# Performance work log

Hardware: AMD Instinct MI355X
Metric: run time of the kernel (lower is better)

## Reference

```python
import jax, jax.numpy as jnp
import numpy as np

D_MODEL = 1024
M = 64            # oscillators; state dim N = 2*M
N = 2 * M
N_H = 2           # Householder reflections per step
DT = 0.1
OMEGA_MAX = 100.0
BATCH, SEQ = 8, 2048


def setup_inputs() -> dict:
    key = jax.random.key(0)
    ks = jax.random.split(key, 8)
    u = jax.random.normal(ks[0], (BATCH, SEQ, D_MODEL), jnp.float32)
    # learned parameters (scaled like the module's small-gain init)
    W_A = jax.random.normal(ks[1], (M, D_MODEL), jnp.float32) * 0.01
    b_A = jnp.zeros((M,), jnp.float32)
    W_k = jax.random.normal(ks[2], (N_H, N, D_MODEL), jnp.float32) * 0.02
    b_k = jnp.zeros((N_H, N), jnp.float32)
    W_beta = jax.random.normal(ks[3], (N_H, D_MODEL), jnp.float32) * 0.02
    b_beta = jnp.zeros((N_H,), jnp.float32)
    B_w = jax.random.normal(ks[4], (N, D_MODEL), jnp.float32) * 0.02
    B_b = jnp.zeros((N,), jnp.float32)
    C = jax.random.normal(ks[5], (D_MODEL, N), jnp.float32) * 0.01
    D = jax.random.normal(ks[6], (D_MODEL,), jnp.float32) * 0.01
    return dict(u=u, W_A=W_A, b_A=b_A, W_k=W_k, b_k=b_k,
                W_beta=W_beta, b_beta=b_beta, B_w=B_w, B_b=B_b, C=C, D=D)


def reference(u, W_A, b_A, W_k, b_k, W_beta, b_beta, B_w, B_b, C, D):
    batch = u.shape[0]
    # --- precompute all input-dependent per-step quantities as big GEMMs ---
    A = jax.nn.relu(jnp.einsum('btd,md->btm', u, W_A) + b_A)
    A = jnp.minimum(A, OMEGA_MAX)                       # clamp(max=omega_max)
    S = 1.0 / (1.0 + (DT * DT) * A)                     # (B,T,M)
    K = jnp.einsum('btd,jnd->btjn', u, W_k) + b_k       # (B,T,n_h,N)
    K = K / jnp.maximum(jnp.linalg.norm(K, axis=-1, keepdims=True), 1e-12)
    beta = 2.0 * jax.nn.sigmoid(jnp.einsum('btd,jd->btj', u, W_beta) + b_beta)
    Bt = jnp.einsum('btd,nd->btn', u, B_w) + B_b        # (B,T,N)

    # time-major for scan
    xs = (jnp.moveaxis(A, 1, 0), jnp.moveaxis(S, 1, 0), jnp.moveaxis(K, 1, 0),
          jnp.moveaxis(beta, 1, 0), jnp.moveaxis(Bt, 1, 0))
    h0 = jnp.zeros((batch, N), u.dtype)

    def step(h, x):
        A_t, S_t, K_t, beta_t, B_t = x
        # oscillatory rotation-contraction R_t @ h (m 2x2 blocks)
        z, y = h[:, :M], h[:, M:]
        z_new = S_t * z - DT * A_t * S_t * y
        y_new = DT * S_t * z + S_t * y
        h = jnp.concatenate([z_new, y_new], axis=-1)
        # sequential Householder product H_t @ h (fixed small n_h loop)
        for j in range(N_H):
            k = K_t[:, j]                                # (B,N), unit norm
            dot = jnp.sum(k * h, axis=-1, keepdims=True)
            h = h - beta_t[:, j:j + 1] * k * dot
        h = h + B_t
        return h, h

    _, hs = jax.lax.scan(step, h0, xs)                  # (T,B,N)
    hs = jnp.moveaxis(hs, 0, 1)                         # (B,T,N)
    return jnp.einsum('btn,dn->btd', hs, C) + u * D
```

## Files before the change

### kernel.cpp

```cpp
#include <hip/hip_runtime.h>
#include <cmath>


#define NTOK 16384
#define TT 2048
#define BB 8
#define DM 1024
#define FS 520
#define CH 64
#define LCH 32
#define NCH 512
#define NW 448
#define NWP 512

typedef short bf16x8 __attribute__((ext_vector_type(8)));
typedef float f32x4 __attribute__((ext_vector_type(4)));

#define GLOAD_LDS16(g, l)                                          \
  __builtin_amdgcn_global_load_lds(                                \
      (const __attribute__((address_space(1))) void*)(g),          \
      (__attribute__((address_space(3))) void*)(l), 16, 0, 0)

#define RAW_BAR() do {                                             \
    asm volatile("s_waitcnt lgkmcnt(0)" ::: "memory");             \
    __builtin_amdgcn_sched_barrier(0);                             \
    __builtin_amdgcn_s_barrier();                                  \
    __builtin_amdgcn_sched_barrier(0);                             \
  } while (0)

#define WAIT_VM(N) do {                                            \
    __builtin_amdgcn_sched_barrier(0);                             \
    asm volatile("s_waitcnt vmcnt(" #N ")" ::: "memory");          \
    __builtin_amdgcn_sched_barrier(0);                             \
  } while (0)

__global__ __launch_bounds__(256) void packW(
    const float* __restrict__ W_A, const float* __restrict__ b_A,
    const float* __restrict__ W_k, const float* __restrict__ b_k,
    const float* __restrict__ b_beta,
    const float* __restrict__ B_w, const float* __restrict__ B_b,
    float* __restrict__ Wp, float* __restrict__ bias) {
  int r = blockIdx.x;
  int tid = threadIdx.x;
  const float* src;
  float bv;
  if (r < 64)       { src = W_A + (size_t)r * DM;         bv = b_A[r]; }
  else if (r < 320) { src = W_k + (size_t)(r - 64) * DM;  bv = b_k[r - 64]; }
  else              { src = B_w + (size_t)(r - 320) * DM; bv = B_b[r - 320]; }
  ((float4*)(Wp + (size_t)r * DM))[tid] = ((const float4*)src)[tid];
  if (tid == 0) bias[r] = bv;
  if (r == 0 && tid < 2) bias[448 + tid] = b_beta[tid];
}

__device__ inline unsigned short bf16_rne(float x) {
  unsigned b = __float_as_uint(x);
  b += 0x7FFFu + ((b >> 16) & 1u);
  return (unsigned short)(b >> 16);
}

__device__ inline void split_bf16(float x, unsigned short& h, unsigned short& l) {
  unsigned b = __float_as_uint(x);
  h = (unsigned short)(b >> 16);
  float rem = x - __uint_as_float(b & 0xFFFF0000u);
  l = bf16_rne(rem);
}

__global__ __launch_bounds__(256) void convertU(
    const float* __restrict__ u, unsigned short* __restrict__ uh,
    unsigned short* __restrict__ ul) {
  int gid = blockIdx.x * 256 + threadIdx.x;
  int m = gid >> 8;
  int g = gid & 255;
  float4 v = *(const float4*)(u + (size_t)m * DM + g * 4);
  int kt = g >> 3, gg = g & 7;
  int p = gg & 3, h = gg >> 2;
  int mr = m & 127, mb = m >> 7;
  int pp = p ^ ((mr >> 2) & 3);
  size_t dst = ((size_t)(mb * 32 + kt)) * 4096 + mr * 32 + ((pp << 1) | h) * 4;
  ushort4 hi, lo;
  split_bf16(v.x, hi.x, lo.x);
  split_bf16(v.y, hi.y, lo.y);
  split_bf16(v.z, hi.z, lo.z);
  split_bf16(v.w, hi.w, lo.w);
  *(ushort4*)(uh + dst) = hi;
  *(ushort4*)(ul + dst) = lo;
}

__global__ __launch_bounds__(256) void convertW(
    const float* __restrict__ Wp, unsigned short* __restrict__ Wb) {
  int gid = blockIdx.x * 256 + threadIdx.x;
  int n = gid >> 8, g = gid & 255;
  int kt = g >> 3, gg = g & 7;
  int p = gg & 3, h = gg >> 2;
  int nr = n & 127, nb = n >> 7;
  int pp = p ^ ((nr >> 2) & 3);
  size_t dst = ((size_t)(nb * 32 + kt)) * 4096 + nr * 32 + ((pp << 1) | h) * 4;
  ushort4 hv = make_ushort4(0, 0, 0, 0);
  if (n < NW) {
    float4 v = *(const float4*)(Wp + (size_t)n * DM + g * 4);
    hv.x = bf16_rne(v.x); hv.y = bf16_rne(v.y);
    hv.z = bf16_rne(v.z); hv.w = bf16_rne(v.w);
  }
  *(ushort4*)(Wb + dst) = hv;
}

__global__ __launch_bounds__(256) void convertC(
    const float* __restrict__ Cm, unsigned short* __restrict__ Chp,
    unsigned short* __restrict__ Clp) {
  int gid = blockIdx.x * 256 + threadIdx.x;
  int d = gid >> 5;
  int g = gid & 31;
  float4 v = *(const float4*)(Cm + (size_t)d * 128 + g * 4);
  int kt = g >> 3, gg = g & 7;
  int p = gg & 3, h = gg >> 2;
  int nr = d & 127, nb = d >> 7;
  int pp = p ^ ((nr >> 2) & 3);
  size_t dst = ((size_t)(nb * 4 + kt)) * 4096 + nr * 32 + ((pp << 1) | h) * 4;
  ushort4 hi, lo;
  split_bf16(v.x, hi.x, lo.x);
  split_bf16(v.y, hi.y, lo.y);
  split_bf16(v.z, hi.z, lo.z);
  split_bf16(v.w, hi.w, lo.w);
  *(ushort4*)(Chp + dst) = hi;
  *(ushort4*)(Clp + dst) = lo;
}

__global__ __launch_bounds__(256) void gemmA_mfma(
    const unsigned short* __restrict__ uh, const unsigned short* __restrict__ ul,
    const unsigned short* __restrict__ Wb, float* __restrict__ Feat) {
  __shared__ __align__(16) unsigned short As[8192];
  __shared__ __align__(16) unsigned short Bs[8192];
  const int tid = threadIdx.x;
  const int wv = tid >> 6, ln = tid & 63;
  const int lr = ln & 15, G = ln >> 4;
  const int wm = wv >> 1, wn = wv & 1;
  const int x = G ^ (lr >> 2);
  f32x4 acc[4][4];
#pragma unroll
  for (int i = 0; i < 4; ++i)
#pragma unroll
    for (int j = 0; j < 4; ++j) acc[i][j] = (f32x4){0.f, 0.f, 0.f, 0.f};

  const size_t aBase = (size_t)blockIdx.x * 32 * 4096;
  const size_t bBase = (size_t)blockIdx.y * 32 * 4096;
  const int so = wv * 512 + ln * 8;
  const int ld = wv * 512;

  auto stage = [&](int step, int buf) {
    const unsigned short* pa = (step < 32) ? uh : ul;
    const int kt = step & 31;
    const unsigned short* ga = pa + aBase + (size_t)kt * 4096;
    const unsigned short* gb = Wb + bBase + (size_t)kt * 4096;
    unsigned short* A = As + buf * 4096;
    unsigned short* B = Bs + buf * 4096;
    GLOAD_LDS16(ga + so,        A + ld);
    GLOAD_LDS16(ga + 2048 + so, A + 2048 + ld);
    GLOAD_LDS16(gb + so,        B + ld);
    GLOAD_LDS16(gb + 2048 + so, B + 2048 + ld);
  };

  stage(0, 0);
  __syncthreads();
  for (int s = 0; s < 64; ++s) {
    const int cur = s & 1;
    if (s + 1 < 64) stage(s + 1, cur ^ 1);
    bf16x8 af[4], bfr[4];
    const char* Ab = (const char*)(As + cur * 4096) + ((wm * 64 + lr) << 6) + (x << 4);
    const char* Bb = (const char*)(Bs + cur * 4096) + ((wn * 64 + lr) << 6) + (x << 4);
#pragma unroll
    for (int i = 0; i < 4; ++i) {
      af[i]  = *(const bf16x8*)(Ab + i * 1024);
      bfr[i] = *(const bf16x8*)(Bb + i * 1024);
    }
#pragma unroll
    for (int i = 0; i < 4; ++i)
#pragma unroll
      for (int j = 0; j < 4; ++j)
        acc[i][j] = __builtin_amdgcn_mfma_f32_16x16x32_bf16(
            af[i], bfr[j], acc[i][j], 0, 0, 0);
    __syncthreads();
  }
  const int row0 = (blockIdx.x << 7) + wm * 64 + (G << 2);
  const int col0 = (blockIdx.y << 7) + wn * 64 + lr;
  float* fb = Feat + (size_t)row0 * FS + col0;
#pragma unroll
  for (int i = 0; i < 4; ++i)
#pragma unroll
    for (int j = 0; j < 4; ++j) {
      float* d = fb + (size_t)(i * 16) * FS + j * 16;
#pragma unroll
      for (int r = 0; r < 4; ++r) d[(size_t)r * FS] = acc[i][j][r];
    }
}

__global__ __launch_bounds__(256) void gemmC_mfma(
    const unsigned short* __restrict__ hsh, const unsigned short* __restrict__ hsl,
    const unsigned short* __restrict__ Chp, const unsigned short* __restrict__ Clp,
    const float* __restrict__ u, const float* __restrict__ Dv,
    float* __restrict__ out) {
  __shared__ __align__(16) unsigned short As[8192];
  __shared__ __align__(16) unsigned short Bs[8192];
  const int tid = threadIdx.x;
  const int wv = tid >> 6, ln = tid & 63;
  const int lr = ln & 15, G = ln >> 4;
  const int wm = wv >> 1, wn = wv & 1;
  const int x = G ^ (lr >> 2);
  f32x4 acc[4][4];
#pragma unroll
  for (int i = 0; i < 4; ++i)
#pragma unroll
    for (int j = 0; j < 4; ++j) acc[i][j] = (f32x4){0.f, 0.f, 0.f, 0.f};

  const size_t aBase = (size_t)blockIdx.x * 4 * 4096;
  const size_t bBase = (size_t)blockIdx.y * 4 * 4096;
  const int so = wv * 512 + ln * 8;
  const int ld = wv * 512;

  auto stage = [&](int step, int buf) {
    const int pass = step >> 2, kt = step & 3;
    const unsigned short* pa = (pass == 1) ? hsl : hsh;
    const unsigned short* pb = (pass == 2) ? Clp : Chp;
    const unsigned short* ga = pa + aBase + (size_t)kt * 4096;
    const unsigned short* gb = pb + bBase + (size_t)kt * 4096;
    unsigned short* A = As + buf * 4096;
    unsigned short* B = Bs + buf * 4096;
    GLOAD_LDS16(ga + so,        A + ld);
    GLOAD_LDS16(ga + 2048 + so, A + 2048 + ld);
    GLOAD_LDS16(gb + so,        B + ld);
    GLOAD_LDS16(gb + 2048 + so, B + 2048 + ld);
  };

  stage(0, 0);
  __syncthreads();
  for (int s = 0; s < 12; ++s) {
    const int cur = s & 1;
    if (s + 1 < 12) stage(s + 1, cur ^ 1);
    bf16x8 af[4], bfr[4];
    const char* Ab = (const char*)(As + cur * 4096) + ((wm * 64 + lr) << 6) + (x << 4);
    const char* Bb = (const char*)(Bs + cur * 4096) + ((wn * 64 + lr) << 6) + (x << 4);
#pragma unroll
    for (int i = 0; i < 4; ++i) {
      af[i]  = *(const bf16x8*)(Ab + i * 1024);
      bfr[i] = *(const bf16x8*)(Bb + i * 1024);
    }
#pragma unroll
    for (int i = 0; i < 4; ++i)
#pragma unroll
      for (int j = 0; j < 4; ++j)
        acc[i][j] = __builtin_amdgcn_mfma_f32_16x16x32_bf16(
            af[i], bfr[j], acc[i][j], 0, 0, 0);
    __syncthreads();
  }
  const int row0 = (blockIdx.x << 7) + wm * 64 + (G << 2);
  const int col0 = (blockIdx.y << 7) + wn * 64 + lr;
#pragma unroll
  for (int j = 0; j < 4; ++j) {
    float dv = Dv[col0 + j * 16];
#pragma unroll
    for (int i = 0; i < 4; ++i) {
#pragma unroll
      for (int r = 0; r < 4; ++r) {
        size_t off = (size_t)(row0 + i * 16 + r) * DM + col0 + j * 16;
        out[off] = fmaf(u[off], dv, acc[i][j][r]);
      }
    }
  }
}

__device__ inline float wave_sum(float v) {
#pragma unroll
  for (int off = 32; off > 0; off >>= 1) v += __shfl_xor(v, off, 64);
  return v;
}

__global__ __launch_bounds__(64) void postA(float* __restrict__ Feat,
                                            const float* __restrict__ bias,
                                            const float* __restrict__ u,
                                            const float* __restrict__ Wb) {
  const int t = blockIdx.x, lane = threadIdx.x;
  float* f = Feat + (size_t)t * FS;
  float s0 = 0.f, s1 = 0.f;
#pragma unroll
  for (int j = 0; j < 4; ++j) {
    float4 uv = *(const float4*)(u + (size_t)t * DM + j * 256 + lane * 4);
    float4 w0 = *(const float4*)(Wb + j * 256 + lane * 4);
    float4 w1 = *(const float4*)(Wb + DM + j * 256 + lane * 4);
    s0 = fmaf(uv.x, w0.x, s0); s0 = fmaf(uv.y, w0.y, s0);
    s0 = fmaf(uv.z, w0.z, s0); s0 = fmaf(uv.w, w0.w, s0);
    s1 = fmaf(uv.x, w1.x, s1); s1 = fmaf(uv.y, w1.y, s1);
    s1 = fmaf(uv.z, w1.z, s1); s1 = fmaf(uv.w, w1.w, s1);
  }
  s0 = wave_sum(s0); s1 = wave_sum(s1);
  float a = f[lane] + bias[lane];
  a = fminf(fmaxf(a, 0.f), 100.f);
  float S = 1.f / (1.f + 0.01f * a);
  f[lane] = S;
  f[448 + lane] = 0.1f * a * S;
  float k10 = f[64 + lane] + bias[64 + lane];
  float k11 = f[128 + lane] + bias[128 + lane];
  float n1 = wave_sum(k10 * k10 + k11 * k11);
  float inv1 = 1.f / fmaxf(sqrtf(n1), 1e-12f);
  k10 *= inv1; k11 *= inv1;
  f[64 + lane] = k10; f[128 + lane] = k11;
  float k20 = f[192 + lane] + bias[192 + lane];
  float k21 = f[256 + lane] + bias[256 + lane];
  float n2 = wave_sum(k20 * k20 + k21 * k21);
  float inv2 = 1.f / fmaxf(sqrtf(n2), 1e-12f);
  k20 *= inv2; k21 *= inv2;
  f[192 + lane] = k20; f[256 + lane] = k21;
  float c12 = wave_sum(k10 * k20 + k11 * k21);
  if (lane == 0) {
    f[512] = 2.f / (1.f + expf(-(s0 + bias[448])));
    f[513] = 2.f / (1.f + expf(-(s1 + bias[449])));
    f[514] = c12;
  }
  f[320 + lane] += bias[320 + lane];
  f[384 + lane] += bias[384 + lane];
}

__global__ __launch_bounds__(1024, 8) void scanB01(
    const float* __restrict__ Feat, float* __restrict__ Mc,
    float* __restrict__ dc) {
  const int bid = blockIdx.x;
  const int tid = threadIdx.x;
  __shared__ float fb[2][4 * FS];

  if (bid < NCH / 16) {
    const int cid = bid * 16 + (tid >> 6);
    const int lane = tid & 63;
    float z = 0.f, y = 0.f;
    const int t0 = (cid >> 6) * TT + (cid & 63) * LCH;
    for (int t = t0; t < t0 + LCH; ++t) {
      const float* __restrict__ f = Feat + (size_t)t * FS;
      float s = f[lane], c1 = f[448 + lane];
      float k1z = f[64 + lane], k1y = f[128 + lane];
      float k2z = f[192 + lane], k2y = f[256 + lane];
      float bz = f[320 + lane], by = f[384 + lane];
      float b1 = f[512], b2 = f[513], c12 = f[514];
      float sz = s * z;
      float zn = fmaf(-c1, y, sz);
      float yn = fmaf(s, y, 0.1f * sz);
      float p = fmaf(k1y, yn, k1z * zn);
      float qq = fmaf(k2y, yn, k2z * zn);
#pragma unroll
      for (int off = 32; off > 0; off >>= 1) {
        p += __shfl_xor(p, off, 64);
        qq += __shfl_xor(qq, off, 64);
      }
      float e1 = b1 * p;
      float d2 = fmaf(-c12, e1, qq);
      float e2 = b2 * d2;
      z = fmaf(-e1, k1z, zn); z = fmaf(-e2, k2z, z); z += bz;
      y = fmaf(-e1, k1y, yn); y = fmaf(-e2, k2y, y); y += by;
    }
    dc[(size_t)cid * 128 + lane] = z;
    dc[(size_t)cid * 128 + 64 + lane] = y;
    return;
  }

  const int cid = bid - NCH / 16;
  const int t0 = (cid >> 6) * TT + (cid & 63) * LCH;
  const int col = tid >> 3, q = tid & 7;
  const int i0 = q * 8;
  float mz[8], my[8];
#pragma unroll
  for (int j = 0; j < 8; ++j) {
    mz[j] = (i0 + j == col) ? 1.f : 0.f;
    my[j] = (64 + i0 + j == col) ? 1.f : 0.f;
  }
  {
    const float4* src = (const float4*)(Feat + (size_t)t0 * FS);
    if (tid < FS) ((float4*)fb[0])[tid] = src[tid];
  }
  __syncthreads();
  for (int g = 0; g < LCH / 4; ++g) {
    const int cur = g & 1;
    float4 pf0;
    const bool pre = (g < LCH / 4 - 1) && (tid < FS);
    if (pre) {
      const float4* src = (const float4*)(Feat + (size_t)(t0 + (g + 1) * 4) * FS);
      pf0 = src[tid];
    }
#pragma unroll
    for (int s = 0; s < 4; ++s) {
      const float* f = fb[cur] + s * FS;
      float sj[8], cj[8], k1z[8], k1y[8], k2z[8], k2y[8];
#pragma unroll
      for (int v = 0; v < 2; ++v) {
        *(float4*)&sj[4 * v]  = *(const float4*)(f + i0 + 4 * v);
        *(float4*)&cj[4 * v]  = *(const float4*)(f + 448 + i0 + 4 * v);
        *(float4*)&k1z[4 * v] = *(const float4*)(f + 64 + i0 + 4 * v);
        *(float4*)&k1y[4 * v] = *(const float4*)(f + 128 + i0 + 4 * v);
        *(float4*)&k2z[4 * v] = *(const float4*)(f + 192 + i0 + 4 * v);
        *(float4*)&k2y[4 * v] = *(const float4*)(f + 256 + i0 + 4 * v);
      }
      float4 sc = *(const float4*)(f + 512);
      float p0 = 0.f, p1 = 0.f, r0 = 0.f, r1 = 0.f;
#pragma unroll
      for (int j = 0; j < 8; ++j) {
        float s0 = sj[j], c1 = cj[j];
        float z = mz[j], y = my[j];
        float sz = s0 * z;
        z = fmaf(-c1, y, sz);
        y = fmaf(s0, y, 0.1f * sz);
        mz[j] = z; my[j] = y;
        if (j & 1) {
          p1 = fmaf(k1z[j], z, p1); p1 = fmaf(k1y[j], y, p1);
          r1 = fmaf(k2z[j], z, r1); r1 = fmaf(k2y[j], y, r1);
        } else {
          p0 = fmaf(k1z[j], z, p0); p0 = fmaf(k1y[j], y, p0);
          r0 = fmaf(k2z[j], z, r0); r0 = fmaf(k2y[j], y, r0);
        }
      }
      float p = p0 + p1, r2 = r0 + r1;
      p  += __shfl_xor(p, 1, 64);  p  += __shfl_xor(p, 2, 64);
      p  += __shfl_xor(p, 4, 64);
      r2 += __shfl_xor(r2, 1, 64); r2 += __shfl_xor(r2, 2, 64);
      r2 += __shfl_xor(r2, 4, 64);
      float e1 = sc.x * p;
      float e2 = sc.y * fmaf(-sc.z, e1, r2);
#pragma unroll
      for (int j = 0; j < 8; ++j) {
        float z = fmaf(-e1, k1z[j], mz[j]);
        mz[j] = fmaf(-e2, k2z[j], z);
        float y = fmaf(-e1, k1y[j], my[j]);
        my[j] = fmaf(-e2, k2y[j], y);
      }
    }
    if (pre) ((float4*)fb[1 - cur])[tid] = pf0;
    __syncthreads();
  }
  float* dst = Mc + ((size_t)cid * 128 + col) * 128;
  *(float4*)(dst + i0)          = *(float4*)&mz[0];
  *(float4*)(dst + i0 + 4)      = *(float4*)&mz[4];
  *(float4*)(dst + 64 + i0)     = *(float4*)&my[0];
  *(float4*)(dst + 64 + i0 + 4) = *(float4*)&my[4];
}

__global__ __launch_bounds__(1024, 1) void scanB2(
    const float* __restrict__ Mc, const float* __restrict__ dc,
    float* __restrict__ hstart) {
  const int b = blockIdx.x;
  const int tid = threadIdx.x;
  const int i = tid & 127, jh = tid >> 7;
  const int wv = tid >> 6;
  __shared__ __align__(16) float Ms[2][16384];
  __shared__ float h[128];
  __shared__ float red[8][128];
  if (tid < 128) h[tid] = 0.f;

  auto stage = [&](int cn, int buf) {
    const float* g = Mc + (size_t)(b * CH + cn) * 16384;
#pragma unroll
    for (int q = 0; q < 4; ++q) {
      const float* gp = g + q * 4096 + wv * 256 + (tid & 63) * 4;
      float* lp = Ms[buf] + q * 4096 + wv * 256;
      GLOAD_LDS16(gp, lp);
    }
  };

  stage(0, 0);
  float d0 = dc[(size_t)(b * CH) * 128 + i];
  __syncthreads();

  int cur = 0;
  for (int c = 0; c < CH; ++c) {
    const int cn = (c + 1) & (CH - 1);
    stage(cn, cur ^ 1);
    float d1 = dc[(size_t)(b * CH + cn) * 128 + i];
    WAIT_VM(5);
    RAW_BAR();
    if (tid < 128) hstart[(size_t)(b * CH + c) * 128 + tid] = h[tid];
    float acc = 0.f;
#pragma unroll
    for (int j = 0; j < 16; ++j)
      acc = fmaf(Ms[cur][(jh * 16 + j) * 128 + i], h[jh * 16 + j], acc);
    red[jh][i] = acc;
    RAW_BAR();
    if (tid < 128) {
      float sum = d0;
#pragma unroll
      for (int k = 0; k < 8; ++k) sum += red[k][tid];
      h[tid] = sum;
    }
    d0 = d1;
    cur ^= 1;
  }
}

__global__ __launch_bounds__(64) void scanB3(
    const float* __restrict__ Feat, const float* __restrict__ hstart,
    unsigned short* __restrict__ hsh, unsigned short* __restrict__ hsl) {
  const int cid = blockIdx.x;
  const int lane = threadIdx.x;
  float z = hstart[(size_t)cid * 128 + lane];
  float y = hstart[(size_t)cid * 128 + 64 + lane];
  const int t0 = (cid >> 6) * TT + (cid & 63) * LCH;
  const int ktz = lane >> 5, kkz = lane & 31;
  const int kty = (64 + lane) >> 5;
  const int pz = (kkz >> 2) & 3, hz = kkz >> 4;
  const int lowz = kkz & 3;
  for (int t = t0; t < t0 + LCH; ++t) {
    const float* __restrict__ f = Feat + (size_t)t * FS;
    float s = f[lane], c1 = f[448 + lane];
    float k1z = f[64 + lane], k1y = f[128 + lane];
    float k2z = f[192 + lane], k2y = f[256 + lane];
    float bz = f[320 + lane], by = f[384 + lane];
    float b1 = f[512], b2 = f[513], c12 = f[514];
    float sz = s * z;
    float zn = fmaf(-c1, y, sz);
    float yn = fmaf(s, y, 0.1f * sz);
    float p = fmaf(k1y, yn, k1z * zn);
    float qq = fmaf(k2y, yn, k2z * zn);
#pragma unroll
    for (int off = 32; off > 0; off >>= 1) {
      p += __shfl_xor(p, off, 64);
      qq += __shfl_xor(qq, off, 64);
    }
    float e1 = b1 * p;
    float d2 = fmaf(-c12, e1, qq);
    float e2 = b2 * d2;
    zn = fmaf(-e1, k1z, zn); zn = fmaf(-e2, k2z, zn); zn += bz;
    yn = fmaf(-e1, k1y, yn); yn = fmaf(-e2, k2y, yn); yn += by;
    {
      const int mb = t >> 7, mr = t & 127;
      const int xr = (mr >> 2) & 3;
      size_t idxz = ((size_t)(mb * 4 + ktz)) * 4096 + mr * 32 +
                    ((((pz ^ xr) << 1) | hz)) * 4 + lowz;
      size_t idxy = ((size_t)(mb * 4 + kty)) * 4096 + mr * 32 +
                    ((((pz ^ xr) << 1) | hz)) * 4 + lowz;
      unsigned short hi, lo;
      split_bf16(zn, hi, lo);
      hsh[idxz] = hi; hsl[idxz] = lo;
      split_bf16(yn, hi, lo);
      hsh[idxy] = hi; hsl[idxy] = lo;
    }
    z = zn; y = yn;
  }
}

extern "C" void kernel_launch(void* const* d_in, const int* in_sizes, int n_in,
                              void* d_out, int out_size, void* d_ws, size_t ws_size,
                              hipStream_t stream) {
  const float* u      = (const float*)d_in[0];
  const float* W_A    = (const float*)d_in[1];
  const float* b_A    = (const float*)d_in[2];
  const float* W_k    = (const float*)d_in[3];
  const float* b_k    = (const float*)d_in[4];
  const float* W_beta = (const float*)d_in[5];
  const float* b_beta = (const float*)d_in[6];
  const float* B_w    = (const float*)d_in[7];
  const float* B_b    = (const float*)d_in[8];
  const float* Cm     = (const float*)d_in[9];
  const float* Dv     = (const float*)d_in[10];
  float* out = (float*)d_out;
  char* ws = (char*)d_ws;
  float* Wp     = (float*)(ws);
  unsigned short* Wb = (unsigned short*)(ws + 1835008);
  float* bias   = (float*)(ws + 4194304);
  float* Feat   = (float*)(ws + 4198400);
  unsigned short* uh = (unsigned short*)(ws + 38277120);
  float* Mc     = (float*)(ws + 38277120);
  unsigned short* ul = (unsigned short*)(ws + 71831552);
  unsigned short* hsh = (unsigned short*)(ws + 71831552);
  unsigned short* hsl = (unsigned short*)(ws + 76025856);
  unsigned short* Chp = (unsigned short*)(ws + 80220160);
  unsigned short* Clp = (unsigned short*)(ws + 80482304);
  float* dcv    = (float*)(ws + 80744448);
  float* hstart = (float*)(ws + 81006592);

  packW<<<dim3(448), dim3(256), 0, stream>>>(W_A, b_A, W_k, b_k, b_beta,
                                             B_w, B_b, Wp, bias);
  convertW<<<dim3(512), dim3(256), 0, stream>>>(Wp, Wb);
  convertU<<<dim3(16384), dim3(256), 0, stream>>>(u, uh, ul);
  gemmA_mfma<<<dim3(128, 4), dim3(256), 0, stream>>>(uh, ul, Wb, Feat);
  convertC<<<dim3(128), dim3(256), 0, stream>>>(Cm, Chp, Clp);
  postA<<<dim3(16384), dim3(64), 0, stream>>>(Feat, bias, u, W_beta);
  scanB01<<<dim3(NCH / 16 + NCH), dim3(1024), 0, stream>>>(Feat, Mc, dcv);
  scanB2<<<dim3(8), dim3(1024), 0, stream>>>(Mc, dcv, hstart);
  scanB3<<<dim3(NCH), dim3(64), 0, stream>>>(Feat, hstart, hsh, hsl);
  gemmC_mfma<<<dim3(128, 8), dim3(256), 0, stream>>>(hsh, hsl, Chp, Clp,
                                                     u, Dv, out);
}
```

Measured before the change: 434.9 us.

## Split chunk-scan into separate matrix and offset kernels with 16 rows per thread

Splits the fused scanB01 kernel into scanB1, which builds the per-chunk transition matrices, and scanB0, which computes the per-chunk offsets, each launched separately. scanB1 now uses 512-thread blocks where each thread owns 16 rows instead of 8. This halves the shuffle reduction depth and the thread count per chunk, at the cost of more registers per thread and a serial accumulation chain. The extra launch for scanB0 serializes work that previously shared one grid, and the higher register pressure may lower occupancy.

```diff
diff --git a/kernel.cpp b/kernel.cpp
--- a/kernel.cpp
+++ b/kernel.cpp
@@ -318,75 +318,40 @@
   f[384 + lane] += bias[384 + lane];
 }
 
-__global__ __launch_bounds__(1024, 8) void scanB01(
-    const float* __restrict__ Feat, float* __restrict__ Mc,
-    float* __restrict__ dc) {
-  const int bid = blockIdx.x;
+__global__ __launch_bounds__(512, 2) void scanB1(
+    const float* __restrict__ Feat, float* __restrict__ Mc) {
+  const int cid = blockIdx.x;
+  const int t0 = (cid >> 6) * TT + (cid & 63) * LCH;
   const int tid = threadIdx.x;
+  const int col = tid >> 2, q = tid & 3;
+  const int i0 = q * 16;
   __shared__ float fb[2][4 * FS];
-
-  if (bid < NCH / 16) {
-    const int cid = bid * 16 + (tid >> 6);
-    const int lane = tid & 63;
-    float z = 0.f, y = 0.f;
-    const int t0 = (cid >> 6) * TT + (cid & 63) * LCH;
-    for (int t = t0; t < t0 + LCH; ++t) {
-      const float* __restrict__ f = Feat + (size_t)t * FS;
-      float s = f[lane], c1 = f[448 + lane];
-      float k1z = f[64 + lane], k1y = f[128 + lane];
-      float k2z = f[192 + lane], k2y = f[256 + lane];
-      float bz = f[320 + lane], by = f[384 + lane];
-      float b1 = f[512], b2 = f[513], c12 = f[514];
-      float sz = s * z;
-      float zn = fmaf(-c1, y, sz);
-      float yn = fmaf(s, y, 0.1f * sz);
-      float p = fmaf(k1y, yn, k1z * zn);
-      float qq = fmaf(k2y, yn, k2z * zn);
-#pragma unroll
-      for (int off = 32; off > 0; off >>= 1) {
-        p += __shfl_xor(p, off, 64);
-        qq += __shfl_xor(qq, off, 64);
-      }
-      float e1 = b1 * p;
-      float d2 = fmaf(-c12, e1, qq);
-      float e2 = b2 * d2;
-      z = fmaf(-e1, k1z, zn); z = fmaf(-e2, k2z, z); z += bz;
-      y = fmaf(-e1, k1y, yn); y = fmaf(-e2, k2y, y); y += by;
-    }
-    dc[(size_t)cid * 128 + lane] = z;
-    dc[(size_t)cid * 128 + 64 + lane] = y;
-    return;
-  }
-
-  const int cid = bid - NCH / 16;
-  const int t0 = (cid >> 6) * TT + (cid & 63) * LCH;
-  const int col = tid >> 3, q = tid & 7;
-  const int i0 = q * 8;
-  float mz[8], my[8];
-#pragma unroll
-  for (int j = 0; j < 8; ++j) {
+  float mz[16], my[16];
+#pragma unroll
+  for (int j = 0; j < 16; ++j) {
     mz[j] = (i0 + j == col) ? 1.f : 0.f;
     my[j] = (64 + i0 + j == col) ? 1.f : 0.f;
   }
   {
     const float4* src = (const float4*)(Feat + (size_t)t0 * FS);
-    if (tid < FS) ((float4*)fb[0])[tid] = src[tid];
+    for (int v = tid; v < FS; v += 512) ((float4*)fb[0])[v] = src[v];
   }
   __syncthreads();
   for (int g = 0; g < LCH / 4; ++g) {
     const int cur = g & 1;
-    float4 pf0;
-    const bool pre = (g < LCH / 4 - 1) && (tid < FS);
-    if (pre) {
+    float4 pf0, pf1;
+    const bool has2 = tid < (FS - 512);
+    if (g < LCH / 4 - 1) {
       const float4* src = (const float4*)(Feat + (size_t)(t0 + (g + 1) * 4) * FS);
       pf0 = src[tid];
+      if (has2) pf1 = src[tid + 512];
     }
 #pragma unroll
     for (int s = 0; s < 4; ++s) {
       const float* f = fb[cur] + s * FS;
-      float sj[8], cj[8], k1z[8], k1y[8], k2z[8], k2y[8];
-#pragma unroll
-      for (int v = 0; v < 2; ++v) {
+      float sj[16], cj[16], k1z[16], k1y[16], k2z[16], k2y[16];
+#pragma unroll
+      for (int v = 0; v < 4; ++v) {
         *(float4*)&sj[4 * v]  = *(const float4*)(f + i0 + 4 * v);
         *(float4*)&cj[4 * v]  = *(const float4*)(f + 448 + i0 + 4 * v);
         *(float4*)&k1z[4 * v] = *(const float4*)(f + 64 + i0 + 4 * v);
@@ -395,46 +360,76 @@
         *(float4*)&k2y[4 * v] = *(const float4*)(f + 256 + i0 + 4 * v);
       }
       float4 sc = *(const float4*)(f + 512);
-      float p0 = 0.f, p1 = 0.f, r0 = 0.f, r1 = 0.f;
-#pragma unroll
-      for (int j = 0; j < 8; ++j) {
+      float p = 0.f, r2 = 0.f;
+#pragma unroll
+      for (int j = 0; j < 16; ++j) {
         float s0 = sj[j], c1 = cj[j];
         float z = mz[j], y = my[j];
         float sz = s0 * z;
         z = fmaf(-c1, y, sz);
         y = fmaf(s0, y, 0.1f * sz);
         mz[j] = z; my[j] = y;
-        if (j & 1) {
-          p1 = fmaf(k1z[j], z, p1); p1 = fmaf(k1y[j], y, p1);
-          r1 = fmaf(k2z[j], z, r1); r1 = fmaf(k2y[j], y, r1);
-        } else {
-          p0 = fmaf(k1z[j], z, p0); p0 = fmaf(k1y[j], y, p0);
-          r0 = fmaf(k2z[j], z, r0); r0 = fmaf(k2y[j], y, r0);
-        }
+        p  = fmaf(k1z[j], z, p);  p  = fmaf(k1y[j], y, p);
+        r2 = fmaf(k2z[j], z, r2); r2 = fmaf(k2y[j], y, r2);
       }
-      float p = p0 + p1, r2 = r0 + r1;
       p  += __shfl_xor(p, 1, 64);  p  += __shfl_xor(p, 2, 64);
-      p  += __shfl_xor(p, 4, 64);
       r2 += __shfl_xor(r2, 1, 64); r2 += __shfl_xor(r2, 2, 64);
-      r2 += __shfl_xor(r2, 4, 64);
       float e1 = sc.x * p;
       float e2 = sc.y * fmaf(-sc.z, e1, r2);
 #pragma unroll
-      for (int j = 0; j < 8; ++j) {
+      for (int j = 0; j < 16; ++j) {
         float z = fmaf(-e1, k1z[j], mz[j]);
         mz[j] = fmaf(-e2, k2z[j], z);
         float y = fmaf(-e1, k1y[j], my[j]);
         my[j] = fmaf(-e2, k2y[j], y);
       }
     }
-    if (pre) ((float4*)fb[1 - cur])[tid] = pf0;
+    if (g < LCH / 4 - 1) {
+      ((float4*)fb[1 - cur])[tid] = pf0;
+      if (has2) ((float4*)fb[1 - cur])[tid + 512] = pf1;
+    }
     __syncthreads();
   }
   float* dst = Mc + ((size_t)cid * 128 + col) * 128;
-  *(float4*)(dst + i0)          = *(float4*)&mz[0];
-  *(float4*)(dst + i0 + 4)      = *(float4*)&mz[4];
-  *(float4*)(dst + 64 + i0)     = *(float4*)&my[0];
-  *(float4*)(dst + 64 + i0 + 4) = *(float4*)&my[4];
+#pragma unroll
+  for (int v = 0; v < 4; ++v)
+    *(float4*)(dst + i0 + 4 * v) = *(float4*)&mz[4 * v];
+#pragma unroll
+  for (int v = 0; v < 4; ++v)
+    *(float4*)(dst + 64 + i0 + 4 * v) = *(float4*)&my[4 * v];
+}
+
+__global__ __launch_bounds__(64) void scanB0(
+    const float* __restrict__ Feat, float* __restrict__ dc) {
+  const int cid = blockIdx.x;
+  const int lane = threadIdx.x;
+  float z = 0.f, y = 0.f;
+  const int t0 = (cid >> 6) * TT + (cid & 63) * LCH;
+  for (int t = t0; t < t0 + LCH; ++t) {
+    const float* __restrict__ f = Feat + (size_t)t * FS;
+    float s = f[lane], c1 = f[448 + lane];
+    float k1z = f[64 + lane], k1y = f[128 + lane];
+    float k2z = f[192 + lane], k2y = f[256 + lane];
+    float bz = f[320 + lane], by = f[384 + lane];
+    float b1 = f[512], b2 = f[513], c12 = f[514];
+    float sz = s * z;
+    float zn = fmaf(-c1, y, sz);
+    float yn = fmaf(s, y, 0.1f * sz);
+    float p = fmaf(k1y, yn, k1z * zn);
+    float qq = fmaf(k2y, yn, k2z * zn);
+#pragma unroll
+    for (int off = 32; off > 0; off >>= 1) {
+      p += __shfl_xor(p, off, 64);
+      qq += __shfl_xor(qq, off, 64);
+    }
+    float e1 = b1 * p;
+    float d2 = fmaf(-c12, e1, qq);
+    float e2 = b2 * d2;
+    z = fmaf(-e1, k1z, zn); z = fmaf(-e2, k2z, z); z += bz;
+    y = fmaf(-e1, k1y, yn); y = fmaf(-e2, k2y, y); y += by;
+  }
+  dc[(size_t)cid * 128 + lane] = z;
+  dc[(size_t)cid * 128 + 64 + lane] = y;
 }
 
 __global__ __launch_bounds__(1024, 1) void scanB2(
@@ -576,7 +571,8 @@
   gemmA_mfma<<<dim3(128, 4), dim3(256), 0, stream>>>(uh, ul, Wb, Feat);
   convertC<<<dim3(128), dim3(256), 0, stream>>>(Cm, Chp, Clp);
   postA<<<dim3(16384), dim3(64), 0, stream>>>(Feat, bias, u, W_beta);
-  scanB01<<<dim3(NCH / 16 + NCH), dim3(1024), 0, stream>>>(Feat, Mc, dcv);
+  scanB1<<<dim3(NCH), dim3(512), 0, stream>>>(Feat, Mc);
+  scanB0<<<dim3(NCH), dim3(64), 0, stream>>>(Feat, dcv);
   scanB2<<<dim3(8), dim3(1024), 0, stream>>>(Mc, dcv, hstart);
   scanB3<<<dim3(NCH), dim3(64), 0, stream>>>(Feat, hstart, hsh, hsl);
   gemmC_mfma<<<dim3(128, 8), dim3(256), 0, stream>>>(hsh, hsl, Chp, Clp,
```

Result: faster. 423.9 us (-2.5%).
